# Performance work log

Measured on AMD Instinct MI355X. Metric: run time of the kernel, lower is better.

Reference implementation:

```python
import jax, jax.numpy as jnp
import numpy as np

T, N, E = 8, 20000, 320000
D_IN, H, OUT = 64, 128, 2
EPS = 1e-5  # BatchNorm eps


def setup_inputs() -> dict:
    key = jax.random.key(0)
    ks = jax.random.split(key, 24)
    rn = lambda k, shape: jax.random.normal(k, shape, jnp.float32) * 0.05
    inp = {
        "x_seq": jax.random.normal(ks[0], (T, N, D_IN), jnp.float32),
        "edge_index_seq": jax.random.randint(ks[1], (T, 2, E), 0, N),
        # GCN layer 1 (D_IN -> H) + BatchNorm (eval mode: running stats)
        "W1": rn(ks[2], (D_IN, H)), "b1": jnp.zeros((H,), jnp.float32),
        "g1": jnp.ones((H,), jnp.float32), "be1": jnp.zeros((H,), jnp.float32),
        "m1": rn(ks[3], (H,)), "v1": jax.random.uniform(ks[4], (H,), jnp.float32, 0.5, 1.5),
        # GCN layer 2 (H -> H) + BatchNorm
        "W2": rn(ks[5], (H, H)), "b2": jnp.zeros((H,), jnp.float32),
        "g2": jnp.ones((H,), jnp.float32), "be2": jnp.zeros((H,), jnp.float32),
        "m2": rn(ks[6], (H,)), "v2": jax.random.uniform(ks[7], (H,), jnp.float32, 0.5, 1.5),
        # LSTM layer 0 (PyTorch layout: W_ih [4H, in], W_hh [4H, H], gate order i,f,g,o)
        "Wih0": rn(ks[8], (4 * H, H)), "Whh0": rn(ks[9], (4 * H, H)),
        "bih0": jnp.zeros((4 * H,), jnp.float32), "bhh0": jnp.zeros((4 * H,), jnp.float32),
        # LSTM layer 1
        "Wih1": rn(ks[10], (4 * H, H)), "Whh1": rn(ks[11], (4 * H, H)),
        "bih1": jnp.zeros((4 * H,), jnp.float32), "bhh1": jnp.zeros((4 * H,), jnp.float32),
        # final classifier
        "Wc": rn(ks[12], (OUT, H)), "bc": jnp.zeros((OUT,), jnp.float32),
    }
    return inp


def gcn_conv(x, src, dst, W, b):
    # GCNConv: D^{-1/2}(A+I)D^{-1/2} X W + b, self-loops added
    n = x.shape[0]
    h = x @ W                                   # [N, F_out]
    loop = jnp.arange(n)
    s = jnp.concatenate([src, loop])
    d = jnp.concatenate([dst, loop])
    deg = jax.ops.segment_sum(jnp.ones(d.shape, x.dtype), d, num_segments=n)
    dinv = jax.lax.rsqrt(deg)                   # deg >= 1 (self-loops)
    coef = dinv[s] * dinv[d]                    # [E+N]
    agg = jax.ops.segment_sum(h[s] * coef[:, None], d, num_segments=n)
    return agg + b


def batchnorm_eval(x, g, b, m, v):
    return (x - m) * jax.lax.rsqrt(v + EPS) * g + b


def lstm_layer(xs, Wih, Whh, b):
    # xs: [T, in]; returns (ys [T,H], h_T [H])
    h0 = jnp.zeros((Whh.shape[1],), xs.dtype)

    def step(carry, xt):
        h, c = carry
        gates = xt @ Wih.T + h @ Whh.T + b
        i, f, g, o = jnp.split(gates, 4, axis=-1)
        c = jax.nn.sigmoid(f) * c + jax.nn.sigmoid(i) * jnp.tanh(g)
        h = jax.nn.sigmoid(o) * jnp.tanh(c)
        return (h, c), h

    (hT, _), ys = jax.lax.scan(step, (h0, h0), xs)
    return ys, hT


def reference(x_seq, edge_index_seq, W1, b1, g1, be1, m1, v1,
              W2, b2, g2, be2, m2, v2,
              Wih0, Whh0, bih0, bhh0, Wih1, Whh1, bih1, bhh1, Wc, bc):
    def per_t(x, e):
        src, dst = e[0], e[1]
        h = gcn_conv(x, src, dst, W1, b1)
        h = jax.nn.relu(batchnorm_eval(h, g1, be1, m1, v1))
        h = gcn_conv(h, src, dst, W2, b2)
        h = batchnorm_eval(h, g2, be2, m2, v2)
        return h.mean(axis=0)                   # global mean pool (batch=None)

    emb = jax.vmap(per_t)(x_seq, edge_index_seq)  # [T, H]
    ys, _ = lstm_layer(emb, Wih0, Whh0, bih0 + bhh0)
    _, hT = lstm_layer(ys, Wih1, Whh1, bih1 + bhh1)
    out = hT @ Wc.T + bc                          # [OUT]
    return (out[None, :], hT[None, :])
```

## Files before the change

### kernel.cpp

```cpp
#include <hip/hip_runtime.h>
#include <hip/hip_fp16.h>
#include <math.h>

#define T 8
#define N 20000
#define E 320000
#define EPS 1e-5f
#define NBA 32
#define CHUNKA 10000
#define NPACK 10000
#define NPACK4 5000
#define TILES_PT 1250
#define BW 625
#define NBUK 32
#define SPAN_MAX 13824
#define CSGRID 157
#define CVTBLK 2500

typedef _Float16 f16x8 __attribute__((ext_vector_type(8)));
typedef float f32x4 __attribute__((ext_vector_type(4)));
struct h2x2 { __half2 lo, hi; };

__device__ __forceinline__ float sigm(float x) { return 1.0f / (1.0f + expf(-x)); }

__global__ __launch_bounds__(1024) void k_partA(const int* __restrict__ edges,
                                                unsigned int* __restrict__ hist_g,
                                                unsigned int* __restrict__ bpart,
                                                int* __restrict__ bcnt) {
    __shared__ unsigned int arr[CHUNKA];
    __shared__ int cnt[NBUK], cur[NBUK];
    const int t = blockIdx.x & 7, b = blockIdx.x >> 3;
    const int tid = threadIdx.x;
    const int* keys = edges + (size_t)t * 2 * E + E + b * CHUNKA;
    const int* pays = edges + (size_t)t * 2 * E + b * CHUNKA;
    for (int i = tid; i < NPACK4; i += 1024) arr[i] = 0;
    if (tid < NBUK) cnt[tid] = 0;
    __syncthreads();
    for (int i = tid; i < CHUNKA; i += 1024) {
        int k = keys[i];
        atomicAdd(&arr[k >> 2], 1u << ((k & 3) * 8));
        atomicAdd(&cnt[k / BW], 1);
    }
    __syncthreads();
    unsigned int* hout = hist_g + (size_t)(t * NBA + b) * NPACK4;
    for (int i = tid; i < NPACK4; i += 1024) hout[i] = arr[i];
    if (tid == 0) {
        int run = 0;
        for (int u = 0; u < NBUK; u++) { cur[u] = run; run += cnt[u]; }
    }
    if (tid < NBUK) bcnt[(t * NBUK + tid) * NBUK + b] = cnt[tid];
    __syncthreads();
    for (int i = tid; i < CHUNKA; i += 1024) {
        int k = keys[i];
        int p = pays[i];
        int slot = atomicAdd(&cur[k / BW], 1);
        arr[slot] = ((unsigned int)k << 15) | (unsigned int)p;
    }
    __syncthreads();
    unsigned int* outp = bpart + (size_t)(t * NBUK + b) * CHUNKA;
    for (int i = tid; i < CHUNKA; i += 1024) outp[i] = arr[i];
}

__global__ __launch_bounds__(256) void k_colsum(
    const unsigned int* __restrict__ hist_g,
    int* __restrict__ dega, float* __restrict__ dinv,
    const float* __restrict__ W1, __half* __restrict__ W1t,
    float* __restrict__ pooled) {
    const int bid = blockIdx.x, tid = threadIdx.x;
    if (bid >= CSGRID) {
        int i = (bid - CSGRID) * 256 + tid;
        int j = i & 127, k = i >> 7;
        W1t[j * 64 + k] = __float2half(W1[i]);
        if (bid == CSGRID) {
            f32x4 z = {0.f, 0.f, 0.f, 0.f};
            ((f32x4*)pooled)[tid] = z;
        }
        return;
    }
    int idx = bid * 256 + tid;
    if (idx >= T * NPACK4) return;
    int t = idx / NPACK4, i = idx - t * NPACK4;
    const unsigned int* hp = hist_g + (size_t)t * NBA * NPACK4 + i;
    unsigned int a0 = 0, a1 = 0, a2 = 0, a3 = 0;
#pragma unroll
    for (int b = 0; b < NBA; b++) {
        unsigned int h = hp[(size_t)b * NPACK4];
        a0 += h & 0xffu; a1 += (h >> 8) & 0xffu;
        a2 += (h >> 16) & 0xffu; a3 += h >> 24;
    }
    int4 dd; dd.x = (int)a0; dd.y = (int)a1; dd.z = (int)a2; dd.w = (int)a3;
    ((int4*)dega)[idx] = dd;
    float4 df;
    df.x = rsqrtf((float)a0 + 1.0f); df.y = rsqrtf((float)a1 + 1.0f);
    df.z = rsqrtf((float)a2 + 1.0f); df.w = rsqrtf((float)a3 + 1.0f);
    ((float4*)dinv)[idx] = df;
}

__global__ __launch_bounds__(1024) void k_scanN(const int* __restrict__ dega,
                                                int* __restrict__ offs) {
    const int t = blockIdx.x, tid = threadIdx.x;
    __shared__ int sh[1024];
    int local[20];
    int sum = 0;
    if (tid < 1000) {
        const int* tp = dega + t * N + tid * 20;
#pragma unroll
        for (int i = 0; i < 20; i++) { local[i] = tp[i]; sum += local[i]; }
    }
    sh[tid] = sum;
    __syncthreads();
    for (int off = 1; off < 1024; off <<= 1) {
        int v = (tid >= off) ? sh[tid - off] : 0;
        __syncthreads();
        sh[tid] += v;
        __syncthreads();
    }
    if (tid < 1000) {
        int run = t * E + sh[tid] - sum;
        int* op = offs + t * N + tid * 20;
#pragma unroll
        for (int i = 0; i < 20; i++) { op[i] = run; run += local[i]; }
    }
    if (t == T - 1 && tid == 0) offs[T * N] = T * E;
}

__global__ __launch_bounds__(1024) void k_pw(const unsigned int* __restrict__ bpart,
                                             const int* __restrict__ bcnt,
                                             const int* __restrict__ offs,
                                             const float* __restrict__ dinv,
                                             int* __restrict__ eidx,
                                             float* __restrict__ wpart,
                                             const float* __restrict__ x,
                                             __half* __restrict__ xh) {
    __shared__ int sbuf[SPAN_MAX];
    __shared__ int cursor[BW];
    __shared__ int offb[NBUK], lenb[NBUK];
    const int bid = blockIdx.x;
    const int tid = threadIdx.x;
    if (bid >= 2 * T * NBUK) {
        int idx = (bid - 2 * T * NBUK) * 1024 + tid;
        if (idx >= T * N * 16) return;
        if (idx < 16) {
            ushort4 z; z.x = 0; z.y = 0; z.z = 0; z.w = 0;
            ((ushort4*)(xh + (size_t)T * N * 64))[idx] = z;
        }
        float d = dinv[idx >> 4];
        f32x4 vv = __builtin_nontemporal_load((const f32x4*)x + idx);
        __half h0 = __float2half(vv.x * d);
        __half h1 = __float2half(vv.y * d);
        __half h2 = __float2half(vv.z * d);
        __half h3 = __float2half(vv.w * d);
        ushort4 pack;
        pack.x = *(unsigned short*)&h0;
        pack.y = *(unsigned short*)&h1;
        pack.z = *(unsigned short*)&h2;
        pack.w = *(unsigned short*)&h3;
        ((ushort4*)xh)[idx] = pack;
        return;
    }
    if (bid >= T * NBUK) {
        float* wf = (float*)sbuf;
        const int bb = bid - T * NBUK;
        const int t = bb & 7, b = bb >> 3;
        const unsigned int* run = bpart + (size_t)(t * NBUK + b) * CHUNKA;
        const float* dv = dinv + t * N;
        for (int half = 0; half < 2; half++) {
            for (int i = tid; i < NPACK; i += 1024) wf[i] = 0.f;
            __syncthreads();
            int lo = half * NPACK;
            for (int i = tid; i < CHUNKA; i += 1024) {
                unsigned int it = run[i];
                int q = (int)(it & 0x7fffu) - lo;
                if (q >= 0 && q < NPACK) atomicAdd(&wf[q], dv[it >> 15]);
            }
            __syncthreads();
            float* out = wpart + (size_t)(t * NBUK + b) * N + lo;
            for (int i = tid; i < NPACK; i += 1024) out[i] = wf[i];
            __syncthreads();
        }
        return;
    }
    const int t = bid & 7, u = bid >> 3;
    const int nodeBase = t * N + u * BW;
    const int dstBase = u * BW;
    const int segStart = offs[nodeBase];
    const int segEnd = offs[nodeBase + BW];
    const int span = segEnd - segStart;
    if (tid < NBUK) {
        int s = 0;
        for (int uu = 0; uu < u; uu++) s += bcnt[(t * NBUK + uu) * NBUK + tid];
        offb[tid] = s;
        lenb[tid] = bcnt[(t * NBUK + u) * NBUK + tid];
    }
    for (int j = tid; j < BW; j += 1024) cursor[j] = offs[nodeBase + j] - segStart;
    __syncthreads();
    if (span <= SPAN_MAX) {
        for (int b = 0; b < NBUK; b++) {
            const unsigned int* src = bpart + (size_t)(t * NBUK + b) * CHUNKA + offb[b];
            int len = lenb[b];
            for (int i = tid; i < len; i += 1024) {
                unsigned int it = src[i];
                int pos = atomicAdd(&cursor[(int)(it >> 15) - dstBase], 1);
                sbuf[pos] = (int)(it & 0x7fffu) << 4;
            }
            __syncthreads();
        }
        int* out = eidx + segStart;
        for (int i = tid; i < span; i += 1024) out[i] = sbuf[i];
    } else {
        for (int b = 0; b < NBUK; b++) {
            const unsigned int* src = bpart + (size_t)(t * NBUK + b) * CHUNKA + offb[b];
            int len = lenb[b];
            for (int i = tid; i < len; i += 1024) {
                unsigned int it = src[i];
                int pos = atomicAdd(&cursor[(int)(it >> 15) - dstBase], 1);
                eidx[segStart + pos] = (int)(it & 0x7fffu) << 4;
            }
            __syncthreads();
        }
    }
}

__global__ __launch_bounds__(256) void k_gather(
    const int* __restrict__ eidx, const int* __restrict__ offs,
    const float* __restrict__ dinv, const __half* __restrict__ xh,
    __half* __restrict__ vh) {
    const int t = blockIdx.x & 7;
    const int n = ((blockIdx.x >> 3) << 2) + (threadIdx.x >> 6);
    const int lane = threadIdx.x & 63;
    const int q = lane & 15, s = lane >> 4;
    if (n >= N) return;
    const int node = t * N + n;
    const int start = offs[node];
    const int end = offs[node + 1];
    const h2x2* xt4 = (const h2x2*)(xh + (size_t)t * N * 64);
    const int zrow = (T - t) * (N * 16);
    float a0 = 0.f, a1 = 0.f, a2 = 0.f, a3 = 0.f;
    for (int bs = start; bs < end; bs += 64) {
        int cnt = end - bs; if (cnt > 64) cnt = 64;
        int idx = zrow;
        if (lane < cnt) idx = __builtin_nontemporal_load(&eidx[bs + lane]);
        __half2 hlo = __float2half2_rn(0.f);
        __half2 hhi = __float2half2_rn(0.f);
        for (int e = 0; e < cnt; e += 16) {
            int o0 = __shfl(idx, e + s),      o1 = __shfl(idx, e + 4 + s);
            int o2 = __shfl(idx, e + 8 + s),  o3 = __shfl(idx, e + 12 + s);
            h2x2 v0 = xt4[o0 + q], v1 = xt4[o1 + q];
            h2x2 v2 = xt4[o2 + q], v3 = xt4[o3 + q];
            __half2 p01l = __hadd2(v0.lo, v1.lo), p23l = __hadd2(v2.lo, v3.lo);
            __half2 p01h = __hadd2(v0.hi, v1.hi), p23h = __hadd2(v2.hi, v3.hi);
            hlo = __hadd2(hlo, __hadd2(p01l, p23l));
            hhi = __hadd2(hhi, __hadd2(p01h, p23h));
        }
        float2 flo = __half22float2(hlo), fhi = __half22float2(hhi);
        a0 += flo.x; a1 += flo.y; a2 += fhi.x; a3 += fhi.y;
    }
    a0 += __shfl_xor(a0, 16); a1 += __shfl_xor(a1, 16);
    a2 += __shfl_xor(a2, 16); a3 += __shfl_xor(a3, 16);
    a0 += __shfl_xor(a0, 32); a1 += __shfl_xor(a1, 32);
    a2 += __shfl_xor(a2, 32); a3 += __shfl_xor(a3, 32);
    if (s == 0) {
        float di = dinv[node];
        h2x2 self = xt4[(n << 4) + q];
        float2 sl = __half22float2(self.lo), sh = __half22float2(self.hi);
        float r0 = di * (a0 + sl.x), r1 = di * (a1 + sl.y);
        float r2 = di * (a2 + sh.x), r3 = di * (a3 + sh.y);
        h2x2 outp;
        outp.lo = __floats2half2_rn(r0, r1);
        outp.hi = __floats2half2_rn(r2, r3);
        ((h2x2*)vh)[(size_t)node * 16 + q] = outp;
    }
}

__global__ __launch_bounds__(256) void k_mfma_pool(
    const __half* __restrict__ vh, const float* __restrict__ wpart,
    const float* __restrict__ dinv, const __half* __restrict__ W1t,
    const float* __restrict__ b1, const float* __restrict__ g1,
    const float* __restrict__ be1, const float* __restrict__ m1,
    const float* __restrict__ v1, float* __restrict__ pooled) {
    const int t = blockIdx.x & 7;
    const int bt = blockIdx.x >> 3;
    const int w = threadIdx.x >> 6, lane = threadIdx.x & 63;
    const int q = lane >> 4, col = lane & 15;
    const size_t tb = (size_t)t * N;

    f16x8 bfr[8][2];
    float sbv[8], stv[8];
#pragma unroll
    for (int jt = 0; jt < 8; jt++) {
        int j = jt * 16 + col;
        float s = g1[j] * rsqrtf(v1[j] + EPS);
        sbv[jt] = s;
        stv[jt] = s * b1[j] + be1[j] - m1[j] * s;
#pragma unroll
        for (int kk = 0; kk < 2; kk++)
            bfr[jt][kk] = *(const f16x8*)(W1t + (size_t)j * 64 + kk * 32 + q * 8);
    }
    float pool8[8];
#pragma unroll
    for (int jt = 0; jt < 8; jt++) pool8[jt] = 0.f;

    for (int i = 0; i < 8; i++) {
        int tau = bt * 32 + w * 8 + i;
        if (tau >= TILES_PT) break;
        int nb = tau * 16;
        const __half* vrow = vh + (tb + nb + col) * 64;
        f16x8 a0 = *(const f16x8*)(vrow + q * 8);
        f16x8 a1 = *(const f16x8*)(vrow + 32 + q * 8);
        float4 dv = ((const float4*)(dinv + tb + nb))[q];
        float4 sv = {0.f, 0.f, 0.f, 0.f};
#pragma unroll 8
        for (int b = 0; b < NBUK; b++) {
            float4 wv = ((const float4*)(wpart + (size_t)(t * NBUK + b) * N + nb))[q];
            sv.x += wv.x; sv.y += wv.y; sv.z += wv.z; sv.w += wv.w;
        }
        float4 af;
        af.x = dv.x * (sv.x + dv.x);
        af.y = dv.y * (sv.y + dv.y);
        af.z = dv.z * (sv.z + dv.z);
        af.w = dv.w * (sv.w + dv.w);
#pragma unroll
        for (int jt = 0; jt < 8; jt++) {
            f32x4 acc = {0.f, 0.f, 0.f, 0.f};
            acc = __builtin_amdgcn_mfma_f32_16x16x32_f16(a0, bfr[jt][0], acc, 0, 0, 0);
            acc = __builtin_amdgcn_mfma_f32_16x16x32_f16(a1, bfr[jt][1], acc, 0, 0, 0);
            float s = sbv[jt], sh = stv[jt];
            pool8[jt] += fmaxf(s * acc[0] + sh, 0.f) * af.x
                       + fmaxf(s * acc[1] + sh, 0.f) * af.y
                       + fmaxf(s * acc[2] + sh, 0.f) * af.z
                       + fmaxf(s * acc[3] + sh, 0.f) * af.w;
        }
    }
#pragma unroll
    for (int jt = 0; jt < 8; jt++) {
        pool8[jt] += __shfl_xor(pool8[jt], 16);
        pool8[jt] += __shfl_xor(pool8[jt], 32);
    }
    if (lane < 16) {
#pragma unroll
        for (int jt = 0; jt < 8; jt++)
            atomicAdd(&pooled[t * 128 + jt * 16 + lane], pool8[jt]);
    }
}

__global__ __launch_bounds__(1024) void k_head(
    const float* __restrict__ pooled,
    const float* __restrict__ W2, const float* __restrict__ b2,
    const float* __restrict__ g2, const float* __restrict__ be2,
    const float* __restrict__ m2, const float* __restrict__ v2,
    const float* __restrict__ Wih0, const float* __restrict__ bih0,
    const float* __restrict__ bhh0, const float* __restrict__ Whh0,
    const float* __restrict__ Wih1, const float* __restrict__ bih1,
    const float* __restrict__ bhh1, const float* __restrict__ Whh1,
    const float* __restrict__ Wc, const float* __restrict__ bc,
    float* __restrict__ out, float* __restrict__ sink) {
    const int tid = threadIdx.x;
    if (blockIdx.x > 0) {
        int bid = blockIdx.x - 1;
        int start = (bid >> 3) * 32768;
        float s = 0.f;
        for (int i = start + tid; i < start + 32768; i += 1024) {
            float v;
            if (i < 65536) v = Whh0[i];
            else if (i < 131072) v = Whh1[i - 65536];
            else if (i < 196608) v = Wih1[i - 131072];
            else v = Wih0[i - 196608];
            s += v;
        }
        sink[bid * 1024 + tid] = s;
        return;
    }
    __shared__ float es[T][128];
    __shared__ float gx[T][512];
    __shared__ float ys[T][128];
    __shared__ float h[128];
    __shared__ float part[1024];
    const int r = tid & 511, hf = tid >> 9;
    float c = 0.f;
    part[tid] = pooled[tid] * (1.0f / N);
    __syncthreads();
    {
        int tt = tid >> 7, j = tid & 127;
        float sc = g2[j] * rsqrtf(v2[j] + EPS);
        float sh = be2[j] - m2[j] * sc;
        const float* pm = &part[tt * 128];
        float dot = 0.f;
#pragma unroll 8
        for (int k = 0; k < 128; k++) dot += pm[k] * W2[k * 128 + j];
        es[tt][j] = sc * (dot + b2[j]) + sh;
    }
    __syncthreads();
    {
        float4 wreg[16];
        const float4* wrow = (const float4*)(Wih0 + r * 128 + hf * 64);
#pragma unroll
        for (int k = 0; k < 16; k++) wreg[k] = wrow[k];
        float bias = (hf == 0) ? (bih0[r] + bhh0[r]) : 0.f;
        for (int t = 0; t < T; t++) {
            const float4* e4 = ((const float4*)es[t]) + hf * 16;
            float dot = bias;
#pragma unroll
            for (int k = 0; k < 16; k++) {
                float4 wv = wreg[k], ev = e4[k];
                dot += wv.x * ev.x + wv.y * ev.y + wv.z * ev.z + wv.w * ev.w;
            }
            part[tid] = dot;
            __syncthreads();
            if (tid < 512) gx[t][tid] = part[tid] + part[512 + tid];
            __syncthreads();
        }
    }
    if (tid < 128) h[tid] = 0.f;
    __syncthreads();
    {
        float4 wreg[16];
        const float4* wrow = (const float4*)(Whh0 + r * 128 + hf * 64);
#pragma unroll
        for (int k = 0; k < 16; k++) wreg[k] = wrow[k];
        for (int t = 0; t < T; t++) {
            const float4* h4 = ((const float4*)h) + hf * 16;
            float dot = 0.f;
#pragma unroll
            for (int k = 0; k < 16; k++) {
                float4 wv = wreg[k], hv = h4[k];
                dot += wv.x * hv.x + wv.y * hv.y + wv.z * hv.z + wv.w * hv.w;
            }
            part[tid] = dot;
            __syncthreads();
            if (tid < 128) {
                float i_ = gx[t][tid]       + part[tid]       + part[512 + tid];
                float f_ = gx[t][128 + tid] + part[128 + tid] + part[640 + tid];
                float g_ = gx[t][256 + tid] + part[256 + tid] + part[768 + tid];
                float o_ = gx[t][384 + tid] + part[384 + tid] + part[896 + tid];
                c = sigm(f_) * c + sigm(i_) * tanhf(g_);
                float hv = sigm(o_) * tanhf(c);
                h[tid] = hv;
                ys[t][tid] = hv;
            }
            __syncthreads();
        }
    }
    {
        float4 wreg[16];
        const float4* wrow = (const float4*)(Wih1 + r * 128 + hf * 64);
#pragma unroll
        for (int k = 0; k < 16; k++) wreg[k] = wrow[k];
        float bias = (hf == 0) ? (bih1[r] + bhh1[r]) : 0.f;
        for (int t = 0; t < T; t++) {
            const float4* y4 = ((const float4*)ys[t]) + hf * 16;
            float dot = bias;
#pragma unroll
            for (int k = 0; k < 16; k++) {
                float4 wv = wreg[k], yv = y4[k];
                dot += wv.x * yv.x + wv.y * yv.y + wv.z * yv.z + wv.w * yv.w;
            }
            part[tid] = dot;
            __syncthreads();
            if (tid < 512) gx[t][tid] = part[tid] + part[512 + tid];
            __syncthreads();
        }
    }
    if (tid < 128) h[tid] = 0.f;
    c = 0.f;
    __syncthreads();
    {
        float4 wreg[16];
        const float4* wrow = (const float4*)(Whh1 + r * 128 + hf * 64);
#pragma unroll
        for (int k = 0; k < 16; k++) wreg[k] = wrow[k];
        for (int t = 0; t < T; t++) {
            const float4* h4 = ((const float4*)h) + hf * 16;
            float dot = 0.f;
#pragma unroll
            for (int k = 0; k < 16; k++) {
                float4 wv = wreg[k], hv = h4[k];
                dot += wv.x * hv.x + wv.y * hv.y + wv.z * hv.z + wv.w * hv.w;
            }
            part[tid] = dot;
            __syncthreads();
            if (tid < 128) {
                float i_ = gx[t][tid]       + part[tid]       + part[512 + tid];
                float f_ = gx[t][128 + tid] + part[128 + tid] + part[640 + tid];
                float g_ = gx[t][256 + tid] + part[256 + tid] + part[768 + tid];
                float o_ = gx[t][384 + tid] + part[384 + tid] + part[896 + tid];
                c = sigm(f_) * c + sigm(i_) * tanhf(g_);
                h[tid] = sigm(o_) * tanhf(c);
            }
            __syncthreads();
        }
    }
    if (tid < 2) {
        float dot = bc[tid];
#pragma unroll 8
        for (int k = 0; k < 128; k++) dot += h[k] * Wc[tid * 128 + k];
        out[tid] = dot;
    }
    if (tid < 128) out[2 + tid] = h[tid];
}

extern "C" void kernel_launch(void* const* d_in, const int* in_sizes, int n_in,
                              void* d_out, int out_size, void* d_ws, size_t ws_size,
                              hipStream_t stream) {
    const float* x    = (const float*)d_in[0];
    const int*   edges= (const int*)d_in[1];
    const float* W1   = (const float*)d_in[2];
    const float* b1   = (const float*)d_in[3];
    const float* g1   = (const float*)d_in[4];
    const float* be1  = (const float*)d_in[5];
    const float* m1   = (const float*)d_in[6];
    const float* v1   = (const float*)d_in[7];
    const float* W2   = (const float*)d_in[8];
    const float* b2   = (const float*)d_in[9];
    const float* g2   = (const float*)d_in[10];
    const float* be2  = (const float*)d_in[11];
    const float* m2   = (const float*)d_in[12];
    const float* v2   = (const float*)d_in[13];
    const float* Wih0 = (const float*)d_in[14];
    const float* Whh0 = (const float*)d_in[15];
    const float* bih0 = (const float*)d_in[16];
    const float* bhh0 = (const float*)d_in[17];
    const float* Wih1 = (const float*)d_in[18];
    const float* Whh1 = (const float*)d_in[19];
    const float* bih1 = (const float*)d_in[20];
    const float* bhh1 = (const float*)d_in[21];
    const float* Wc   = (const float*)d_in[22];
    const float* bc   = (const float*)d_in[23];

    char* base = (char*)d_ws;
    unsigned int* hist_g = (unsigned int*)base;
    unsigned int* bpart  = (unsigned int*)(base + (size_t)T * NBA * NPACK * 4);
    __half*       vh     = (__half*)base;
    char* p = base + (size_t)T * NBA * NPACK * 4 + (size_t)T * NBUK * CHUNKA * 4;
    __half* xh   = (__half*)p;              p += (size_t)T * N * 64 * 2 + 128;
    int*   offs  = (int*)p;                 p += (size_t)(T * N + 1) * 4 + 12;
    int*   dega  = (int*)p;                 p += (size_t)T * N * 4;
    float* dinv  = (float*)p;               p += (size_t)T * N * 4;
    float* spare = (float*)p;               p += (size_t)T * N * 4;
    float* sink  = (float*)p;               p += (size_t)T * N * 4;
    int*   eidx  = (int*)p;                 p += (size_t)T * E * 4;
    float* wpart = (float*)p;               p += (size_t)T * NBUK * N * 4;
    int*   bcnt  = (int*)p;                 p += (size_t)T * NBUK * NBUK * 4;
    float* pooled= (float*)p;               p += (size_t)T * 128 * 4;
    __half* W1t  = (__half*)p;
    (void)spare;

    k_partA<<<T * NBUK, 1024, 0, stream>>>(edges, hist_g, bpart, bcnt);
    k_colsum<<<CSGRID + 32, 256, 0, stream>>>(hist_g, dega, dinv, W1, W1t, pooled);
    k_scanN<<<T, 1024, 0, stream>>>(dega, offs);
    k_pw<<<2 * T * NBUK + CVTBLK, 1024, 0, stream>>>(bpart, bcnt, offs, dinv,
                                                     eidx, wpart, x, xh);
    k_gather<<<(T * N) / 4, 256, 0, stream>>>(eidx, offs, dinv, xh, vh);
    k_mfma_pool<<<8 * 40, 256, 0, stream>>>(vh, wpart, dinv, W1t, b1, g1, be1, m1, v1, pooled);
    k_head<<<65, 1024, 0, stream>>>(pooled, W2, b2, g2, be2, m2, v2,
                                    Wih0, bih0, bhh0, Whh0, Wih1, bih1, bhh1, Whh1,
                                    Wc, bc, (float*)d_out, sink);
}
```

Measured before the change: 364.1 us.

## Split LSTM head into parallel embedding kernel and fp16-weight recurrent kernel

The single-block head kernel is split in two. A multi-block kernel computes the per-timestep GCN layer-2 projection and the layer-0 input gates in parallel across T blocks, while extra blocks convert the recurrent and layer-1 input LSTM weights to fp16. The serial single-block kernel then reads these half-precision weights from global/L2 inside each step instead of holding fp32 weights in registers, replacing the old cache-warming sink blocks. This adds a kernel launch and lowers weight precision, which risks accuracy drift and extra global reads in the serial loop.

```diff
diff --git a/kernel.cpp b/kernel.cpp
--- a/kernel.cpp
+++ b/kernel.cpp
@@ -343,87 +343,82 @@
     }
 }
 
-__global__ __launch_bounds__(1024) void k_head(
+__global__ __launch_bounds__(512) void k_emb(
     const float* __restrict__ pooled,
     const float* __restrict__ W2, const float* __restrict__ b2,
     const float* __restrict__ g2, const float* __restrict__ be2,
     const float* __restrict__ m2, const float* __restrict__ v2,
     const float* __restrict__ Wih0, const float* __restrict__ bih0,
-    const float* __restrict__ bhh0, const float* __restrict__ Whh0,
-    const float* __restrict__ Wih1, const float* __restrict__ bih1,
-    const float* __restrict__ bhh1, const float* __restrict__ Whh1,
+    const float* __restrict__ bhh0, float* __restrict__ gx0_g,
+    const float* __restrict__ Whh0, const float* __restrict__ Whh1,
+    const float* __restrict__ Wih1,
+    __half* __restrict__ Whh0h, __half* __restrict__ Whh1h,
+    __half* __restrict__ Wih1h) {
+    const int tid = threadIdx.x;
+    if (blockIdx.x >= T) {
+        int wb = blockIdx.x - T;
+        const float* src; __half* dst;
+        if (wb < 16)      { src = Whh0; dst = Whh0h; }
+        else if (wb < 32) { src = Whh1; dst = Whh1h; wb -= 16; }
+        else              { src = Wih1; dst = Wih1h; wb -= 32; }
+        int off = wb * 4096;
+        for (int i = off + tid; i < off + 4096; i += 512)
+            dst[i] = __float2half(src[i]);
+        return;
+    }
+    const int t = blockIdx.x;
+    __shared__ float pm[128];
+    __shared__ float es[128];
+    if (tid < 128) pm[tid] = pooled[t * 128 + tid] * (1.0f / N);
+    __syncthreads();
+    if (tid < 128) {
+        float s = g2[tid] * rsqrtf(v2[tid] + EPS);
+        float sh = be2[tid] - m2[tid] * s;
+        float dot = 0.f;
+#pragma unroll 8
+        for (int k = 0; k < 128; k++) dot += pm[k] * W2[k * 128 + tid];
+        es[tid] = s * (dot + b2[tid]) + sh;
+    }
+    __syncthreads();
+    float dot = bih0[tid] + bhh0[tid];
+    const float4* w = (const float4*)(Wih0 + tid * 128);
+    const float4* e4 = (const float4*)es;
+#pragma unroll
+    for (int k4 = 0; k4 < 32; k4++) {
+        float4 a = w[k4], bb = e4[k4];
+        dot += a.x * bb.x + a.y * bb.y + a.z * bb.z + a.w * bb.w;
+    }
+    gx0_g[t * 512 + tid] = dot;
+}
+
+__global__ __launch_bounds__(1024) void k_head2(
+    const float* __restrict__ gx0_g,
+    const __half* __restrict__ Whh0h, const __half* __restrict__ Wih1h,
+    const __half* __restrict__ Whh1h,
+    const float* __restrict__ bih1, const float* __restrict__ bhh1,
     const float* __restrict__ Wc, const float* __restrict__ bc,
-    float* __restrict__ out, float* __restrict__ sink) {
-    const int tid = threadIdx.x;
-    if (blockIdx.x > 0) {
-        int bid = blockIdx.x - 1;
-        int start = (bid >> 3) * 32768;
-        float s = 0.f;
-        for (int i = start + tid; i < start + 32768; i += 1024) {
-            float v;
-            if (i < 65536) v = Whh0[i];
-            else if (i < 131072) v = Whh1[i - 65536];
-            else if (i < 196608) v = Wih1[i - 131072];
-            else v = Wih0[i - 196608];
-            s += v;
-        }
-        sink[bid * 1024 + tid] = s;
-        return;
-    }
-    __shared__ float es[T][128];
+    float* __restrict__ out) {
     __shared__ float gx[T][512];
     __shared__ float ys[T][128];
     __shared__ float h[128];
     __shared__ float part[1024];
+    const int tid = threadIdx.x;
     const int r = tid & 511, hf = tid >> 9;
     float c = 0.f;
-    part[tid] = pooled[tid] * (1.0f / N);
+    for (int i = tid; i < T * 512; i += 1024) gx[i >> 9][i & 511] = gx0_g[i];
+    if (tid < 128) h[tid] = 0.f;
     __syncthreads();
     {
-        int tt = tid >> 7, j = tid & 127;
-        float sc = g2[j] * rsqrtf(v2[j] + EPS);
-        float sh = be2[j] - m2[j] * sc;
-        const float* pm = &part[tt * 128];
-        float dot = 0.f;
-#pragma unroll 8
-        for (int k = 0; k < 128; k++) dot += pm[k] * W2[k * 128 + j];
-        es[tt][j] = sc * (dot + b2[j]) + sh;
-    }
-    __syncthreads();
-    {
-        float4 wreg[16];
-        const float4* wrow = (const float4*)(Wih0 + r * 128 + hf * 64);
-#pragma unroll
-        for (int k = 0; k < 16; k++) wreg[k] = wrow[k];
-        float bias = (hf == 0) ? (bih0[r] + bhh0[r]) : 0.f;
-        for (int t = 0; t < T; t++) {
-            const float4* e4 = ((const float4*)es[t]) + hf * 16;
-            float dot = bias;
-#pragma unroll
-            for (int k = 0; k < 16; k++) {
-                float4 wv = wreg[k], ev = e4[k];
-                dot += wv.x * ev.x + wv.y * ev.y + wv.z * ev.z + wv.w * ev.w;
-            }
-            part[tid] = dot;
-            __syncthreads();
-            if (tid < 512) gx[t][tid] = part[tid] + part[512 + tid];
-            __syncthreads();
-        }
-    }
-    if (tid < 128) h[tid] = 0.f;
-    __syncthreads();
-    {
-        float4 wreg[16];
-        const float4* wrow = (const float4*)(Whh0 + r * 128 + hf * 64);
-#pragma unroll
-        for (int k = 0; k < 16; k++) wreg[k] = wrow[k];
+        const h2x2* wrow = (const h2x2*)(Whh0h + r * 128 + hf * 64);
         for (int t = 0; t < T; t++) {
             const float4* h4 = ((const float4*)h) + hf * 16;
             float dot = 0.f;
 #pragma unroll
             for (int k = 0; k < 16; k++) {
-                float4 wv = wreg[k], hv = h4[k];
-                dot += wv.x * hv.x + wv.y * hv.y + wv.z * hv.z + wv.w * hv.w;
+                h2x2 wv = wrow[k];
+                float4 hv = h4[k];
+                float2 wl = __half22float2(wv.lo), wh = __half22float2(wv.hi);
+                dot += wl.x * hv.x + wl.y * hv.y + wh.x * hv.z + wh.y * hv.w;
             }
             part[tid] = dot;
             __syncthreads();
@@ -441,18 +436,17 @@
         }
     }
     {
-        float4 wreg[16];
-        const float4* wrow = (const float4*)(Wih1 + r * 128 + hf * 64);
-#pragma unroll
-        for (int k = 0; k < 16; k++) wreg[k] = wrow[k];
+        const h2x2* wrow = (const h2x2*)(Wih1h + r * 128 + hf * 64);
         float bias = (hf == 0) ? (bih1[r] + bhh1[r]) : 0.f;
         for (int t = 0; t < T; t++) {
             const float4* y4 = ((const float4*)ys[t]) + hf * 16;
             float dot = bias;
 #pragma unroll
             for (int k = 0; k < 16; k++) {
-                float4 wv = wreg[k], yv = y4[k];
-                dot += wv.x * yv.x + wv.y * yv.y + wv.z * yv.z + wv.w * yv.w;
+                h2x2 wv = wrow[k];
+                float4 yv = y4[k];
+                float2 wl = __half22float2(wv.lo), wh = __half22float2(wv.hi);
+                dot += wl.x * yv.x + wl.y * yv.y + wh.x * yv.z + wh.y * yv.w;
             }
             part[tid] = dot;
             __syncthreads();
@@ -464,17 +458,16 @@
     c = 0.f;
     __syncthreads();
     {
-        float4 wreg[16];
-        const float4* wrow = (const float4*)(Whh1 + r * 128 + hf * 64);
-#pragma unroll
-        for (int k = 0; k < 16; k++) wreg[k] = wrow[k];
+        const h2x2* wrow = (const h2x2*)(Whh1h + r * 128 + hf * 64);
         for (int t = 0; t < T; t++) {
             const float4* h4 = ((const float4*)h) + hf * 16;
             float dot = 0.f;
 #pragma unroll
             for (int k = 0; k < 16; k++) {
-                float4 wv = wreg[k], hv = h4[k];
-                dot += wv.x * hv.x + wv.y * hv.y + wv.z * hv.z + wv.w * hv.w;
+                h2x2 wv = wrow[k];
+                float4 hv = h4[k];
+                float2 wl = __half22float2(wv.lo), wh = __half22float2(wv.hi);
+                dot += wl.x * hv.x + wl.y * hv.y + wh.x * hv.z + wh.y * hv.w;
             }
             part[tid] = dot;
             __syncthreads();
@@ -531,18 +524,19 @@
     unsigned int* bpart  = (unsigned int*)(base + (size_t)T * NBA * NPACK * 4);
     __half*       vh     = (__half*)base;
     char* p = base + (size_t)T * NBA * NPACK * 4 + (size_t)T * NBUK * CHUNKA * 4;
-    __half* xh   = (__half*)p;              p += (size_t)T * N * 64 * 2 + 128;
-    int*   offs  = (int*)p;                 p += (size_t)(T * N + 1) * 4 + 12;
-    int*   dega  = (int*)p;                 p += (size_t)T * N * 4;
-    float* dinv  = (float*)p;               p += (size_t)T * N * 4;
-    float* spare = (float*)p;               p += (size_t)T * N * 4;
-    float* sink  = (float*)p;               p += (size_t)T * N * 4;
-    int*   eidx  = (int*)p;                 p += (size_t)T * E * 4;
-    float* wpart = (float*)p;               p += (size_t)T * NBUK * N * 4;
-    int*   bcnt  = (int*)p;                 p += (size_t)T * NBUK * NBUK * 4;
-    float* pooled= (float*)p;               p += (size_t)T * 128 * 4;
-    __half* W1t  = (__half*)p;
-    (void)spare;
+    __half* xh    = (__half*)p;             p += (size_t)T * N * 64 * 2 + 128;
+    int*   offs   = (int*)p;                p += (size_t)(T * N + 1) * 4 + 12;
+    int*   dega   = (int*)p;                p += (size_t)T * N * 4;
+    float* dinv   = (float*)p;              p += (size_t)T * N * 4;
+    __half* Whh0h = (__half*)p;             p += (size_t)65536 * 2;
+    __half* Whh1h = (__half*)p;             p += (size_t)65536 * 2;
+    __half* Wih1h = (__half*)p;             p += (size_t)65536 * 2;
+    float* gx0_g  = (float*)p;              p += (size_t)T * 512 * 4;
+    int*   eidx   = (int*)p;                p += (size_t)T * E * 4;
+    float* wpart  = (float*)p;              p += (size_t)T * NBUK * N * 4;
+    int*   bcnt   = (int*)p;                p += (size_t)T * NBUK * NBUK * 4;
+    float* pooled = (float*)p;              p += (size_t)T * 128 * 4;
+    __half* W1t   = (__half*)p;
 
     k_partA<<<T * NBUK, 1024, 0, stream>>>(edges, hist_g, bpart, bcnt);
     k_colsum<<<CSGRID + 32, 256, 0, stream>>>(hist_g, dega, dinv, W1, W1t, pooled);
@@ -551,7 +545,9 @@
                                                      eidx, wpart, x, xh);
     k_gather<<<(T * N) / 4, 256, 0, stream>>>(eidx, offs, dinv, xh, vh);
     k_mfma_pool<<<8 * 40, 256, 0, stream>>>(vh, wpart, dinv, W1t, b1, g1, be1, m1, v1, pooled);
-    k_head<<<65, 1024, 0, stream>>>(pooled, W2, b2, g2, be2, m2, v2,
-                                    Wih0, bih0, bhh0, Whh0, Wih1, bih1, bhh1, Whh1,
-                                    Wc, bc, (float*)d_out, sink);
-}
+    k_emb<<<T + 48, 512, 0, stream>>>(pooled, W2, b2, g2, be2, m2, v2,
+                                      Wih0, bih0, bhh0, gx0_g,
+                                      Whh0, Whh1, Wih1, Whh0h, Whh1h, Wih1h);
+    k_head2<<<1, 1024, 0, stream>>>(gx0_g, Whh0h, Wih1h, Whh1h,
+                                    bih1, bhh1, Wc, bc, (float*)d_out);
+}
```

Measured after the change: 344.5 us. -5.4%, faster.
